# Kernel tuning notes

Hardware: AMD Instinct MI355X
Metric: run time of the kernel (lower is better)

## Reference

```python
import jax, jax.numpy as jnp
import numpy as np

B, L, D = 2, 2048, 1024
H = 16
DH = D // H  # 64


def rope_tables(seq_len, dim):
    # inv_freq: [dim/2]
    inv_freq = 1.0 / (10000.0 ** (jnp.arange(0, dim, 2, dtype=jnp.float32) / dim))
    t = jnp.arange(seq_len, dtype=jnp.float32)
    freqs = jnp.outer(t, inv_freq)            # [L, dim/2]
    emb = jnp.concatenate([freqs, freqs], -1)  # [L, dim]
    return jnp.cos(emb), jnp.sin(emb)


def rotate_half(x):
    x1, x2 = x[..., : x.shape[-1] // 2], x[..., x.shape[-1] // 2 :]
    return jnp.concatenate([-x2, x1], axis=-1)


def setup_inputs() -> dict:
    key = jax.random.key(0)
    k1, k2, k3 = jax.random.split(key, 3)
    x = jax.random.normal(k1, (B, L, D), dtype=jnp.float32)
    # nn.Linear weight init scale ~ 1/sqrt(fan_in)
    Wqkv = jax.random.normal(k2, (D, 3 * D), dtype=jnp.float32) / np.sqrt(D)
    Wo = jax.random.normal(k3, (D, D), dtype=jnp.float32) / np.sqrt(D)
    return {"x": x, "Wqkv": Wqkv, "Wo": Wo}


def reference(x, Wqkv, Wo):
    b, l, d = x.shape
    qkv = (x @ Wqkv).reshape(b, l, 3, H, DH)
    q, k, v = qkv[:, :, 0], qkv[:, :, 1], qkv[:, :, 2]  # [B, L, H, DH]

    cos, sin = rope_tables(l, DH)          # [L, DH]
    cos = cos[:, None, :]                   # [L, 1, DH] broadcast over heads
    sin = sin[:, None, :]
    q = q * cos + rotate_half(q) * sin
    k = k * cos + rotate_half(k) * sin

    scale = DH ** -0.5
    # full (non-causal) attention, faithful to the source
    scores = jnp.einsum("bqhd,bkhd->bhqk", q, k) * scale   # [B, H, L, L]
    attn = jax.nn.softmax(scores, axis=-1)
    out = jnp.einsum("bhqk,bkhd->bqhd", attn, v)            # [B, L, H, DH]
    out = out.reshape(b, l, d)
    return out @ Wo
```

## Files before the change

### kernel.cpp

```cpp
#include <hip/hip_runtime.h>
#include <hip/hip_bf16.h>

#define B_  2
#define L_  2048
#define D_  1024
#define H_  16
#define DH_ 64
#define M_  (B_*L_)
#define N1_ (3*D_)

#define QSCALE (0.125f * 1.44269504088896340736f)

typedef __bf16 bf16x8 __attribute__((ext_vector_type(8)));
typedef float  f32x4  __attribute__((ext_vector_type(4)));
typedef unsigned short ushort_t;
typedef unsigned short ushort8_t __attribute__((ext_vector_type(8)));
typedef unsigned int   uintx2    __attribute__((ext_vector_type(2)));

#define MFMA16(a,b,c) __builtin_amdgcn_mfma_f32_16x16x32_bf16((a),(b),(c),0,0,0)

__device__ __forceinline__ float4 ld4(const float* p) { return *(const float4*)p; }

__device__ __forceinline__ ushort_t f2bf(float f) {
    union { float f; unsigned int u; } v; v.f = f;
    unsigned int r = (v.u + 0x7FFFu + ((v.u >> 16) & 1u)) >> 16;
    return (ushort_t)r;
}
__device__ __forceinline__ float bf2f(ushort_t u) {
    union { unsigned int u; float f; } v; v.u = ((unsigned int)u) << 16;
    return v.f;
}
__device__ __forceinline__ float exp2_(float x) {
    float r; asm("v_exp_f32 %0, %1" : "=v"(r) : "v"(x)); return r;
}
__device__ __forceinline__ float fract_(float x) {
    float r; asm("v_fract_f32 %0, %1" : "=v"(r) : "v"(x)); return r;
}
__device__ __forceinline__ float sin_rev(float x) {
    float r; asm("v_sin_f32 %0, %1" : "=v"(r) : "v"(x)); return r;
}
__device__ __forceinline__ float cos_rev(float x) {
    float r; asm("v_cos_f32 %0, %1" : "=v"(r) : "v"(x)); return r;
}
__device__ __forceinline__ unsigned cvtpk(float a, float b) {
    unsigned r; asm("v_cvt_pk_bf16_f32 %0, %1, %2" : "=v"(r) : "v"(a), "v"(b)); return r;
}
__device__ __forceinline__ float bperm_f(int byte_addr, float v) {
    union { float f; int i; } u; u.f = v;
    u.i = __builtin_amdgcn_ds_bpermute(byte_addr, u.i);
    return u.f;
}
__device__ __forceinline__ void gload16(const ushort_t* g, ushort_t* l) {
    __builtin_amdgcn_global_load_lds(
        (const __attribute__((address_space(1))) unsigned int*)g,
        (__attribute__((address_space(3))) unsigned int*)l, 16, 0, 0);
}

__global__ __launch_bounds__(256)
void convert_x(const float* __restrict__ in, ushort_t* __restrict__ out)
{
    int i = (blockIdx.x * 256 + threadIdx.x) * 8;
    float4 a = ld4(in + i), b = ld4(in + i + 4);
    ushort8_t o;
    o[0] = f2bf(a.x); o[1] = f2bf(a.y); o[2] = f2bf(a.z); o[3] = f2bf(a.w);
    o[4] = f2bf(b.x); o[5] = f2bf(b.y); o[6] = f2bf(b.z); o[7] = f2bf(b.w);
    *(ushort8_t*)(out + i) = o;
}

template<int N>
__global__ __launch_bounds__(256)
void transpose_w(const float* __restrict__ in, ushort_t* __restrict__ out)
{
    __shared__ float vs[64][65];
    const int nt = blockIdx.x, kt = blockIdx.y, t = threadIdx.x;
    #pragma unroll
    for (int i = 0; i < 4; ++i) {
        int idx = t + 256 * i;
        int row = idx >> 4, c4 = idx & 15;
        float4 x4 = ld4(in + (size_t)(kt * 64 + row) * N + nt * 64 + c4 * 4);
        vs[row][c4*4+0] = x4.x; vs[row][c4*4+1] = x4.y;
        vs[row][c4*4+2] = x4.z; vs[row][c4*4+3] = x4.w;
    }
    __syncthreads();
    #pragma unroll
    for (int i = 0; i < 16; ++i) {
        int idx = t + 256 * i;
        int nc = idx >> 6, kc = idx & 63;
        out[(size_t)(nt * 64 + nc) * 1024 + kt * 64 + kc] = f2bf(vs[kc][nc]);
    }
}

template<int EPI, int BM>
__global__ __launch_bounds__(256)
void bgemm(const ushort_t* __restrict__ A, const ushort_t* __restrict__ Bt,
           float* __restrict__ Cf,
           ushort_t* __restrict__ Qo, ushort_t* __restrict__ Ko, ushort_t* __restrict__ Vo)
{
    constexpr int K  = 1024;
    constexpr int MI = BM / 32;
    __shared__ ushort_t As[BM * 64];
    __shared__ ushort_t Bs[128 * 64];
    const int t  = threadIdx.x;
    const int l  = t & 63, w = t >> 6;
    const int g  = l >> 4, ln = l & 15;
    const int wr = w >> 1, wc = w & 1;
    const int m0 = blockIdx.y * BM, n0 = blockIdx.x * 128;

    const int srow = w * 8 + (l >> 3);
    const int sch  = (l & 7) ^ (l >> 3);
    const ushort_t* Ag = A  + ((size_t)(m0 + srow)) * K + sch * 8;
    const ushort_t* Bg = Bt + ((size_t)(n0 + srow)) * K + sch * 8;

    f32x4 acc[MI][4];
    #pragma unroll
    for (int mi = 0; mi < MI; ++mi)
        #pragma unroll
        for (int nj = 0; nj < 4; ++nj) acc[mi][nj] = f32x4{0.f, 0.f, 0.f, 0.f};

    for (int kt = 0; kt < K / 64; ++kt) {
        #pragma unroll
        for (int i = 0; i < BM / 32; ++i)
            gload16(Ag + (size_t)i * 32 * K + kt * 64, &As[i * 2048 + w * 512]);
        #pragma unroll
        for (int i = 0; i < 4; ++i)
            gload16(Bg + (size_t)i * 32 * K + kt * 64, &Bs[i * 2048 + w * 512]);
        __syncthreads();

        #pragma unroll
        for (int kk = 0; kk < 2; ++kk) {
            bf16x8 af[MI], bfv[4];
            #pragma unroll
            for (int mi = 0; mi < MI; ++mi) {
                int row  = (BM / 2) * wr + 16 * mi + ln;
                int phys = (4 * kk + g) ^ (ln & 7);
                af[mi] = *(const bf16x8*)&As[row * 64 + phys * 8];
            }
            #pragma unroll
            for (int nj = 0; nj < 4; ++nj) {
                int row  = 64 * wc + 16 * nj + ln;
                int phys = (4 * kk + g) ^ (ln & 7);
                bfv[nj] = *(const bf16x8*)&Bs[row * 64 + phys * 8];
            }
            #pragma unroll
            for (int mi = 0; mi < MI; ++mi)
                #pragma unroll
                for (int nj = 0; nj < 4; ++nj)
                    acc[mi][nj] = MFMA16(af[mi], bfv[nj], acc[mi][nj]);
        }
        __syncthreads();
    }

    if (EPI == 0) {
        #pragma unroll
        for (int mi = 0; mi < MI; ++mi) {
            #pragma unroll
            for (int nj = 0; nj < 4; ++nj) {
                int n = n0 + 64 * wc + 16 * nj + ln;
                #pragma unroll
                for (int r = 0; r < 4; ++r) {
                    int m = m0 + (BM / 2) * wr + 16 * mi + 4 * g + r;
                    Cf[(size_t)m * D_ + n] = acc[mi][nj][r];
                }
            }
        }
    } else {
        const int nb    = n0 + 64 * wc;
        const int which = nb >> 10;
        const int h     = (nb >> 6) & (H_ - 1);
        if (which == 2) {
            #pragma unroll
            for (int mi = 0; mi < MI; ++mi)
                #pragma unroll
                for (int nj = 0; nj < 4; ++nj) {
                    int dh = 16 * nj + ln;
                    #pragma unroll
                    for (int r = 0; r < 4; ++r) {
                        int m = m0 + (BM / 2) * wr + 16 * mi + 4 * g + r;
                        int b = m >> 11, ll = m & (L_ - 1);
                        Vo[((size_t)(b * H_ + h) * DH_ + dh) * L_ + ll] = f2bf(acc[mi][nj][r]);
                    }
                }
        } else {
            ushort_t* base = (which == 0) ? Qo : Ko;
            const float scale = (which == 0) ? QSCALE : 1.0f;
            const float invr0 = exp2_(-(float)ln        * 0.41524101186f) * 0.15915494310f;
            const float invr1 = exp2_(-(float)(16 + ln) * 0.41524101186f) * 0.15915494310f;
            #pragma unroll
            for (int mi = 0; mi < MI; ++mi) {
                #pragma unroll
                for (int r = 0; r < 4; ++r) {
                    int m = m0 + (BM / 2) * wr + 16 * mi + 4 * g + r;
                    int b = m >> 11, ll = m & (L_ - 1);
                    float rv0 = fract_((float)ll * invr0);
                    float rv1 = fract_((float)ll * invr1);
                    float s0 = sin_rev(rv0), c0 = cos_rev(rv0);
                    float s1 = sin_rev(rv1), c1 = cos_rev(rv1);
                    size_t rb = ((size_t)(b * H_ + h) * L_ + ll) * DH_;
                    float a1 = acc[mi][0][r], a2 = acc[mi][2][r];
                    base[rb + ln]      = f2bf((a1 * c0 - a2 * s0) * scale);
                    base[rb + ln + 32] = f2bf((a2 * c0 + a1 * s0) * scale);
                    float b1 = acc[mi][1][r], b2 = acc[mi][3][r];
                    base[rb + 16 + ln]      = f2bf((b1 * c1 - b2 * s1) * scale);
                    base[rb + 16 + ln + 32] = f2bf((b2 * c1 + b1 * s1) * scale);
                }
            }
        }
    }
}

__global__ __launch_bounds__(256)
void attn_mfma(const ushort_t* __restrict__ qb, const ushort_t* __restrict__ kb,
               const ushort_t* __restrict__ vt, ushort_t* __restrict__ ao)
{
    __shared__ ushort_t Ks[128 * 64];
    __shared__ ushort_t Vs[64 * 128];
    __shared__ ushort_t Ps[4][32 * 64];

    const int t    = threadIdx.x;
    const int lane = t & 63, wv = t >> 6;
    const int g    = lane >> 4, ln = lane & 15;
    const int bh   = blockIdx.x;
    const int q0   = blockIdx.y * 128 + wv * 32;

    const ushort_t* qpA = qb + ((size_t)bh * L_ + q0 + ln) * DH_;
    bf16x8 qf[2][2];
    qf[0][0] = *(const bf16x8*)(qpA + 8 * g);
    qf[0][1] = *(const bf16x8*)(qpA + 32 + 8 * g);
    qf[1][0] = *(const bf16x8*)(qpA + 16 * DH_ + 8 * g);
    qf[1][1] = *(const bf16x8*)(qpA + 16 * DH_ + 32 + 8 * g);

    const ushort_t* kp = kb + (size_t)bh * L_ * DH_;
    const ushort_t* vp = vt + (size_t)bh * DH_ * L_;

    const int krow8 = lane >> 3;
    const int ksch  = (lane & 7) ^ krow8;
    const int vrow4 = lane >> 4;

    char* Pw = (char*)&Ps[wv][0];
    const int swz = (ln & 7) << 4;

    f32x4 O[2][4];
    #pragma unroll
    for (int h = 0; h < 2; ++h)
        #pragma unroll
        for (int n = 0; n < 4; ++n) O[h][n] = f32x4{0.f, 0.f, 0.f, 0.f};
    float m_q[2] = {-INFINITY, -INFINITY}, l_q[2] = {0.f, 0.f};

    auto stage = [&](int tt) {
        #pragma unroll
        for (int i = 0; i < 4; ++i) {
            int row = 32 * wv + 8 * i + krow8;
            gload16(kp + ((size_t)(tt * 128 + row)) * 64 + ksch * 8,
                    &Ks[(32 * wv + 8 * i) * 64]);
        }
        #pragma unroll
        for (int i = 0; i < 4; ++i) {
            int row  = 16 * wv + 4 * i + vrow4;
            int vsch = (lane & 15) ^ ((4 * i + vrow4) & 7);
            gload16(vp + ((size_t)row) * L_ + tt * 128 + vsch * 8,
                    &Vs[(16 * wv + 4 * i) * 128]);
        }
    };

    auto process = [&](int sub) {
        f32x4 S[2][4];
        #pragma unroll
        for (int h = 0; h < 2; ++h)
            #pragma unroll
            for (int n = 0; n < 4; ++n) S[h][n] = f32x4{0.f, 0.f, 0.f, 0.f};
        #pragma unroll
        for (int kk = 0; kk < 2; ++kk) {
            bf16x8 kfv[4];
            #pragma unroll
            for (int n = 0; n < 4; ++n) {
                int row  = 64 * sub + 16 * n + ln;
                int phys = (4 * kk + g) ^ (ln & 7);
                kfv[n] = *(const bf16x8*)&Ks[row * 64 + phys * 8];
            }
            __builtin_amdgcn_s_setprio(1);
            #pragma unroll
            for (int n = 0; n < 4; ++n) S[0][n] = MFMA16(kfv[n], qf[0][kk], S[0][n]);
            #pragma unroll
            for (int n = 0; n < 4; ++n) S[1][n] = MFMA16(kfv[n], qf[1][kk], S[1][n]);
            __builtin_amdgcn_s_setprio(0);
        }

        #pragma unroll
        for (int h = 0; h < 2; ++h) {
            float pmax;
            {
                float a0 = fmaxf(fmaxf(S[h][0][0], S[h][0][1]), fmaxf(S[h][0][2], S[h][0][3]));
                float a1 = fmaxf(fmaxf(S[h][1][0], S[h][1][1]), fmaxf(S[h][1][2], S[h][1][3]));
                float a2 = fmaxf(fmaxf(S[h][2][0], S[h][2][1]), fmaxf(S[h][2][2], S[h][2][3]));
                float a3 = fmaxf(fmaxf(S[h][3][0], S[h][3][1]), fmaxf(S[h][3][2], S[h][3][3]));
                pmax = fmaxf(fmaxf(a0, a1), fmaxf(a2, a3));
            }
            pmax = fmaxf(pmax, __shfl_xor(pmax, 16));
            pmax = fmaxf(pmax, __shfl_xor(pmax, 32));

            if (!__all(pmax - m_q[h] <= 8.0f)) {
                float mnew = fmaxf(m_q[h], pmax);
                float al   = exp2_(m_q[h] - mnew);
                m_q[h] = mnew;
                l_q[h] *= al;
                #pragma unroll
                for (int r = 0; r < 4; ++r) {
                    float alr = bperm_f((4 * g + r) * 4, al);
                    #pragma unroll
                    for (int n = 0; n < 4; ++n) O[h][n][r] *= alr;
                }
            }

            float psum = 0.f;
            #pragma unroll
            for (int n = 0; n < 4; ++n) {
                float p0 = exp2_(S[h][n][0] - m_q[h]);
                float p1 = exp2_(S[h][n][1] - m_q[h]);
                float p2 = exp2_(S[h][n][2] - m_q[h]);
                float p3 = exp2_(S[h][n][3] - m_q[h]);
                psum += (p0 + p1) + (p2 + p3);
                uintx2 wq;
                wq[0] = cvtpk(p0, p1);
                wq[1] = cvtpk(p2, p3);
                *(uintx2*)(Pw + 2048 * h + 128 * ln + ((32 * n + 8 * g) ^ swz)) = wq;
            }
            psum += __shfl_xor(psum, 16);
            psum += __shfl_xor(psum, 32);
            l_q[h] += psum;
        }

        #pragma unroll
        for (int kk = 0; kk < 2; ++kk) {
            bf16x8 vfv[4];
            #pragma unroll
            for (int n = 0; n < 4; ++n) {
                int row  = 16 * n + ln;
                int phys = 8 * sub + ((4 * kk + g) ^ (ln & 7));
                vfv[n] = *(const bf16x8*)&Vs[row * 128 + phys * 8];
            }
            bf16x8 pa0 = *(const bf16x8*)(Pw + 128 * ln + ((64 * kk + 16 * g) ^ swz));
            bf16x8 pa1 = *(const bf16x8*)(Pw + 2048 + 128 * ln + ((64 * kk + 16 * g) ^ swz));
            __builtin_amdgcn_s_setprio(1);
            #pragma unroll
            for (int n = 0; n < 4; ++n) O[0][n] = MFMA16(pa0, vfv[n], O[0][n]);
            #pragma unroll
            for (int n = 0; n < 4; ++n) O[1][n] = MFMA16(pa1, vfv[n], O[1][n]);
            __builtin_amdgcn_s_setprio(0);
        }
    };

    for (int tt = 0; tt < L_ / 128; ++tt) {
        stage(tt);
        __syncthreads();
        process(0);
        process(1);
        __syncthreads();
    }

    const int b = bh >> 4, hh = bh & 15;
    #pragma unroll
    for (int h = 0; h < 2; ++h) {
        #pragma unroll
        for (int r = 0; r < 4; ++r) {
            float lb  = bperm_f((4 * g + r) * 4, l_q[h]);
            float inv = 1.0f / lb;
            int ql = q0 + 16 * h + 4 * g + r;
            ushort_t* dst = ao + ((size_t)(b * L_ + ql)) * D_ + hh * 64;
            #pragma unroll
            for (int n = 0; n < 4; ++n)
                dst[16 * n + ln] = f2bf(O[h][n][r] * inv);
        }
    }
}

extern "C" void kernel_launch(void* const* d_in, const int* in_sizes, int n_in,
                              void* d_out, int out_size, void* d_ws, size_t ws_size,
                              hipStream_t stream)
{
    const float* x    = (const float*)d_in[0];
    const float* Wqkv = (const float*)d_in[1];
    const float* Wo   = (const float*)d_in[2];
    float* out = (float*)d_out;

    char* ws = (char*)d_ws;
    ushort_t* xb  = (ushort_t*)(ws);
    ushort_t* wqt = (ushort_t*)(ws + ((size_t) 8 << 20));
    ushort_t* wot = (ushort_t*)(ws + ((size_t)14 << 20));
    ushort_t* qR  = (ushort_t*)(ws + ((size_t)16 << 20));
    ushort_t* kR  = (ushort_t*)(ws + ((size_t)24 << 20));
    ushort_t* vt  = (ushort_t*)(ws + ((size_t)32 << 20));
    ushort_t* ao  = xb;

    convert_x<<<(M_ * D_) / (8 * 256), 256, 0, stream>>>(x, xb);
    transpose_w<N1_><<<dim3(N1_ / 64, 16), 256, 0, stream>>>(Wqkv, wqt);
    transpose_w<D_ ><<<dim3(D_  / 64, 16), 256, 0, stream>>>(Wo, wot);

    bgemm<1, 128><<<dim3(N1_ / 128, M_ / 128), 256, 0, stream>>>(xb, wqt, nullptr, qR, kR, vt);
    attn_mfma<<<dim3(B_ * H_, L_ / 128), 256, 0, stream>>>(qR, kR, vt, ao);
    bgemm<0, 64><<<dim3(D_ / 128, M_ / 64), 256, 0, stream>>>(ao, wot, out, nullptr, nullptr, nullptr);
}
```

Measured before the change: 137.0 us.

## Fuse prep kernels and fold softmax bias and row-sum into MFMAs

Merges the x conversion and the two weight transposes into a single prep launch, which removes two kernel launches. In attention, the running max is folded into the initial value of the S accumulator so the per-element subtract disappears. The row sum is computed by an extra MFMA of P against a ones vector rather than by VALU adds and cross-lane shuffles. This adds MFMA work per tile, and the row sum now comes from bf16-rounded P values, which slightly changes numerics.

Measured after the change: 129.5 us. 1.06x faster.

```diff
diff --git a/kernel.cpp b/kernel.cpp
--- a/kernel.cpp
+++ b/kernel.cpp
@@ -57,22 +57,30 @@
 }
 
 __global__ __launch_bounds__(256)
-void convert_x(const float* __restrict__ in, ushort_t* __restrict__ out)
-{
-    int i = (blockIdx.x * 256 + threadIdx.x) * 8;
-    float4 a = ld4(in + i), b = ld4(in + i + 4);
-    ushort8_t o;
-    o[0] = f2bf(a.x); o[1] = f2bf(a.y); o[2] = f2bf(a.z); o[3] = f2bf(a.w);
-    o[4] = f2bf(b.x); o[5] = f2bf(b.y); o[6] = f2bf(b.z); o[7] = f2bf(b.w);
-    *(ushort8_t*)(out + i) = o;
-}
-
-template<int N>
-__global__ __launch_bounds__(256)
-void transpose_w(const float* __restrict__ in, ushort_t* __restrict__ out)
+void prep(const float* __restrict__ x, const float* __restrict__ Wqkv,
+          const float* __restrict__ Wo,
+          ushort_t* __restrict__ xb, ushort_t* __restrict__ wqt,
+          ushort_t* __restrict__ wot)
 {
     __shared__ float vs[64][65];
-    const int nt = blockIdx.x, kt = blockIdx.y, t = threadIdx.x;
+    const int bid = blockIdx.x, t = threadIdx.x;
+    if (bid < 2048) {
+        int i = (bid * 256 + t) * 8;
+        float4 a = ld4(x + i), b = ld4(x + i + 4);
+        ushort8_t o;
+        o[0] = f2bf(a.x); o[1] = f2bf(a.y); o[2] = f2bf(a.z); o[3] = f2bf(a.w);
+        o[4] = f2bf(b.x); o[5] = f2bf(b.y); o[6] = f2bf(b.z); o[7] = f2bf(b.w);
+        *(ushort8_t*)(xb + i) = o;
+        return;
+    }
+    const float* in; ushort_t* out; int nt, kt, N;
+    if (bid < 2048 + 768) {
+        in = Wqkv; out = wqt; N = N1_;
+        nt = (bid - 2048) % 48; kt = (bid - 2048) / 48;
+    } else {
+        in = Wo; out = wot; N = D_;
+        nt = (bid - 2816) % 16; kt = (bid - 2816) / 16;
+    }
     #pragma unroll
     for (int i = 0; i < 4; ++i) {
         int idx = t + 256 * i;
@@ -232,6 +240,11 @@
     const ushort_t* kp = kb + (size_t)bh * L_ * DH_;
     const ushort_t* vp = vt + (size_t)bh * DH_ * L_;
 
+    union { ushort8_t u; bf16x8 v; } onesu;
+    #pragma unroll
+    for (int j = 0; j < 8; ++j) onesu.u[j] = 0x3F80;
+    const bf16x8 onesf = onesu.v;
+
     const int krow8 = lane >> 3;
     const int ksch  = (lane & 7) ^ krow8;
     const int vrow4 = lane >> 4;
@@ -239,12 +252,14 @@
     char* Pw = (char*)&Ps[wv][0];
     const int swz = (ln & 7) << 4;
 
-    f32x4 O[2][4];
-    #pragma unroll
-    for (int h = 0; h < 2; ++h)
+    f32x4 O[2][4], lacc[2];
+    #pragma unroll
+    for (int h = 0; h < 2; ++h) {
+        lacc[h] = f32x4{0.f, 0.f, 0.f, 0.f};
         #pragma unroll
         for (int n = 0; n < 4; ++n) O[h][n] = f32x4{0.f, 0.f, 0.f, 0.f};
-    float m_q[2] = {-INFINITY, -INFINITY}, l_q[2] = {0.f, 0.f};
+    }
+    float m_q[2] = {0.f, 0.f};
 
     auto stage = [&](int tt) {
         #pragma unroll
@@ -267,7 +282,8 @@
         #pragma unroll
         for (int h = 0; h < 2; ++h)
             #pragma unroll
-            for (int n = 0; n < 4; ++n) S[h][n] = f32x4{0.f, 0.f, 0.f, 0.f};
+            for (int n = 0; n < 4; ++n)
+                S[h][n] = f32x4{-m_q[h], -m_q[h], -m_q[h], -m_q[h]};
         #pragma unroll
         for (int kk = 0; kk < 2; ++kk) {
             bf16x8 kfv[4];
@@ -298,35 +314,31 @@
             pmax = fmaxf(pmax, __shfl_xor(pmax, 16));
             pmax = fmaxf(pmax, __shfl_xor(pmax, 32));
 
-            if (!__all(pmax - m_q[h] <= 8.0f)) {
-                float mnew = fmaxf(m_q[h], pmax);
-                float al   = exp2_(m_q[h] - mnew);
-                m_q[h] = mnew;
-                l_q[h] *= al;
+            if (!__all(pmax <= 8.0f)) {
+                m_q[h] += pmax;
+                float al = exp2_(-pmax);
                 #pragma unroll
                 for (int r = 0; r < 4; ++r) {
                     float alr = bperm_f((4 * g + r) * 4, al);
+                    lacc[h][r] *= alr;
                     #pragma unroll
                     for (int n = 0; n < 4; ++n) O[h][n][r] *= alr;
                 }
-            }
-
-            float psum = 0.f;
+                #pragma unroll
+                for (int n = 0; n < 4; ++n) S[h][n] = S[h][n] - pmax;
+            }
+
             #pragma unroll
             for (int n = 0; n < 4; ++n) {
-                float p0 = exp2_(S[h][n][0] - m_q[h]);
-                float p1 = exp2_(S[h][n][1] - m_q[h]);
-                float p2 = exp2_(S[h][n][2] - m_q[h]);
-                float p3 = exp2_(S[h][n][3] - m_q[h]);
-                psum += (p0 + p1) + (p2 + p3);
+                float p0 = exp2_(S[h][n][0]);
+                float p1 = exp2_(S[h][n][1]);
+                float p2 = exp2_(S[h][n][2]);
+                float p3 = exp2_(S[h][n][3]);
                 uintx2 wq;
                 wq[0] = cvtpk(p0, p1);
                 wq[1] = cvtpk(p2, p3);
                 *(uintx2*)(Pw + 2048 * h + 128 * ln + ((32 * n + 8 * g) ^ swz)) = wq;
             }
-            psum += __shfl_xor(psum, 16);
-            psum += __shfl_xor(psum, 32);
-            l_q[h] += psum;
         }
 
         #pragma unroll
@@ -345,6 +357,8 @@
             for (int n = 0; n < 4; ++n) O[0][n] = MFMA16(pa0, vfv[n], O[0][n]);
             #pragma unroll
             for (int n = 0; n < 4; ++n) O[1][n] = MFMA16(pa1, vfv[n], O[1][n]);
+            lacc[0] = MFMA16(pa0, onesf, lacc[0]);
+            lacc[1] = MFMA16(pa1, onesf, lacc[1]);
             __builtin_amdgcn_s_setprio(0);
         }
     };
@@ -362,8 +376,7 @@
     for (int h = 0; h < 2; ++h) {
         #pragma unroll
         for (int r = 0; r < 4; ++r) {
-            float lb  = bperm_f((4 * g + r) * 4, l_q[h]);
-            float inv = 1.0f / lb;
+            float inv = 1.0f / lacc[h][r];
             int ql = q0 + 16 * h + 4 * g + r;
             ushort_t* dst = ao + ((size_t)(b * L_ + ql)) * D_ + hh * 64;
             #pragma unroll
@@ -391,10 +404,7 @@
     ushort_t* vt  = (ushort_t*)(ws + ((size_t)32 << 20));
     ushort_t* ao  = xb;
 
-    convert_x<<<(M_ * D_) / (8 * 256), 256, 0, stream>>>(x, xb);
-    transpose_w<N1_><<<dim3(N1_ / 64, 16), 256, 0, stream>>>(Wqkv, wqt);
-    transpose_w<D_ ><<<dim3(D_  / 64, 16), 256, 0, stream>>>(Wo, wot);
-
+    prep<<<3072, 256, 0, stream>>>(x, Wqkv, Wo, xb, wqt, wot);
     bgemm<1, 128><<<dim3(N1_ / 128, M_ / 128), 256, 0, stream>>>(xb, wqt, nullptr, qR, kR, vt);
     attn_mfma<<<dim3(B_ * H_, L_ / 128), 256, 0, stream>>>(qR, kR, vt, ao);
     bgemm<0, 64><<<dim3(D_ / 128, M_ / 64), 256, 0, stream>>>(ao, wot, out, nullptr, nullptr, nullptr);
```
